# Optimization experiments

Hardware: AMD Instinct MI355X
Metric: run time of the kernel (lower is better)

## Reference

```python
import jax, jax.numpy as jnp
import numpy as np

N = 35          # nodes (hardcoded by x.repeat(35,1,1))
V = 4           # edge views
D1, D2, D3 = 512, 256, 128


def _full_graph_edges():
    # fully connected, no self loops, COO [2, E], E = 35*34
    src, dst = np.meshgrid(np.arange(N), np.arange(N), indexing='ij')
    mask = src != dst
    return np.stack([src[mask], dst[mask]], axis=0).astype(np.int64)


def setup_inputs() -> dict:
    key = jax.random.key(0)
    ks = jax.random.split(key, 8)
    E = N * (N - 1)
    edge_index = jnp.asarray(_full_graph_edges())
    s1, s2, s3 = 1.0 / np.sqrt(V), 1.0 / np.sqrt(V), 1.0 / np.sqrt(V)
    return {
        'x': jnp.ones((N, 1), jnp.float32),
        'edge_attr': jax.random.uniform(ks[0], (E, V), jnp.float32),
        'edge_index': edge_index,
        'mlp1_w': jax.random.normal(ks[1], (V, 1 * D1), jnp.float32) * s1,
        'mlp1_b': jnp.zeros((1 * D1,), jnp.float32),
        'root1': jax.random.normal(ks[2], (1, D1), jnp.float32),
        'bias1': jnp.zeros((D1,), jnp.float32),
        'mlp2_w': jax.random.normal(ks[3], (V, D1 * D2), jnp.float32) * s2,
        'mlp2_b': jnp.zeros((D1 * D2,), jnp.float32),
        'root2': jax.random.normal(ks[4], (D1, D2), jnp.float32) / np.sqrt(D1),
        'bias2': jnp.zeros((D2,), jnp.float32),
        'mlp3_w': jax.random.normal(ks[5], (V, D2 * D3), jnp.float32) * s3,
        'mlp3_b': jnp.zeros((D2 * D3,), jnp.float32),
        'root3': jax.random.normal(ks[6], (D2, D3), jnp.float32) / np.sqrt(D2),
        'bias3': jnp.zeros((D3,), jnp.float32),
    }


def _nnconv(x, edge_attr, src, dst, mlp_w, mlp_b, root, bias, in_c, out_c):
    # edge MLP -> per-edge weight matrix [E, in_c, out_c]
    w = jax.nn.relu(edge_attr @ mlp_w + mlp_b).reshape(-1, in_c, out_c)
    # gather source feats, per-edge matmul: [E, out_c]
    msg = jnp.einsum('ei,eio->eo', x[src], w)
    # scatter-mean to targets
    agg = jax.ops.segment_sum(msg, dst, num_segments=N)
    cnt = jax.ops.segment_sum(jnp.ones_like(msg[:, 0]), dst, num_segments=N)
    agg = agg / jnp.maximum(cnt, 1.0)[:, None]
    return agg + x @ root + bias


def reference(x, edge_attr, edge_index, mlp1_w, mlp1_b, root1, bias1,
              mlp2_w, mlp2_b, root2, bias2, mlp3_w, mlp3_b, root3, bias3):
    src, dst = edge_index[0], edge_index[1]
    h = jax.nn.relu(_nnconv(x, edge_attr, src, dst, mlp1_w, mlp1_b, root1, bias1, 1, D1))
    h = jax.nn.relu(_nnconv(h, edge_attr, src, dst, mlp2_w, mlp2_b, root2, bias2, D1, D2))
    h = jax.nn.relu(_nnconv(h, edge_attr, src, dst, mlp3_w, mlp3_b, root3, bias3, D2, D3))
    # cbt[a, i] = sum_f |h[i, f] - h[a, f]|   (repeat / transpose / abs / sum)
    cbt = jnp.sum(jnp.abs(h[None, :, :] - h[:, None, :]), axis=2)
    return cbt
```

## Files before the change

kernel.cpp:

```cpp
#include <hip/hip_runtime.h>

#define NN 35

typedef float v2f __attribute__((ext_vector_type(2)));

__device__ __forceinline__ v2f pk_fma(v2f a, v2f b, v2f c) {
#if __has_builtin(__builtin_elementwise_fma)
    return __builtin_elementwise_fma(a, b, c);
#else
    v2f d; d.x = fmaf(a.x, b.x, c.x); d.y = fmaf(a.y, b.y, c.y); return d;
#endif
}
__device__ __forceinline__ v2f pk_relu(v2f a) {
    v2f d; d.x = fmaxf(a.x, 0.f); d.y = fmaxf(a.y, 0.f); return d;
}
__device__ __forceinline__ v2f pk_splat(float s) { v2f d; d.x = s; d.y = s; return d; }
__device__ __forceinline__ v2f pk_make(float a, float b) { v2f d; d.x = a; d.y = b; return d; }

__device__ __forceinline__ void agst(float* p, float v) {
    __hip_atomic_store(p, v, __ATOMIC_RELAXED, __HIP_MEMORY_SCOPE_AGENT);
}


__global__ __launch_bounds__(256, 2)
void edge12_kernel(const float* __restrict__ x,
                   const float* __restrict__ ea,
                   const float* __restrict__ W1, const float* __restrict__ b1,
                   const float* __restrict__ root1, const float* __restrict__ bias1,
                   const float* __restrict__ W2, const float* __restrict__ b2,
                   const float* __restrict__ root2,
                   float* __restrict__ part,
                   float* __restrict__ agg3)
{
    const int d  = blockIdx.x;
    const int c  = blockIdx.y;
    const int i0 = c * 8;
    const int o  = threadIdx.x;
    const int bid = c * 35 + d;

    __shared__ __align__(16) float hs[35][8];
    __shared__ float4 as[34];
    __shared__ float xs[NN];

    if (bid < 18) {
        const int zi = bid * 256 + o;
        if (zi < 35 * 128) agst(&agg3[zi], 0.f);
    }

    v2f Wv0[4], Wv1[4], Wv2[4], Wv3[4], BB[4], RR[4];
#pragma unroll
    for (int p = 0; p < 4; ++p) {
        const size_t b0 = (size_t)(i0 + 2 * p) * 256 + o;
        const size_t bq = b0 + 256;
        Wv0[p] = pk_make(W2[b0],          W2[bq]);
        Wv1[p] = pk_make(W2[131072 + b0], W2[131072 + bq]);
        Wv2[p] = pk_make(W2[262144 + b0], W2[262144 + bq]);
        Wv3[p] = pk_make(W2[393216 + b0], W2[393216 + bq]);
        BB[p]  = pk_make(b2[b0],          b2[bq]);
        RR[p]  = pk_make(root2[b0],       root2[bq]);
    }

    if (o < NN) xs[o] = x[o];
    if (o >= 70 && o < 104) {
        const int j = o - 70;
        const int s = j + (j >= d ? 1 : 0);
        as[j] = ((const float4*)ea)[s * 34 + (d < s ? d : d - 1)];
    }
    __syncthreads();

    for (int e = o; e < 280; e += 256) {
        const int s = e >> 3, ii = e & 7, i = i0 + ii;
        const float w0 = W1[i], w1 = W1[512 + i], w2 = W1[1024 + i], w3 = W1[1536 + i];
        const float bb = b1[i];
        float sum = 0.f;
#pragma unroll
        for (int t = 0; t < NN; ++t) {
            if (t == s) continue;
            const float4 a = ((const float4*)ea)[t * 34 + (s < t ? s : s - 1)];
            float w = fmaf(a.x, w0, fmaf(a.y, w1, fmaf(a.z, w2, fmaf(a.w, w3, bb))));
            sum = fmaf(xs[t], fmaxf(w, 0.f), sum);
        }
        hs[s][ii] = fmaxf(sum * (1.f / 34.f) + xs[s] * root1[i] + bias1[i], 0.f);
    }
    __syncthreads();

    v2f acc0 = pk_splat(0.f), acc1 = pk_splat(0.f);
#pragma unroll 2
    for (int j = 0; j < 34; ++j) {
        const int sj = j + (j >= d ? 1 : 0);
        const float4 a = as[j];
        const v2f ax = pk_splat(a.x), ay = pk_splat(a.y);
        const v2f az = pk_splat(a.z), aw = pk_splat(a.w);
#pragma unroll
        for (int k = 0; k < 2; ++k) {
            const float4 hv = ((const float4*)hs[sj])[k];
            {
                const int p = k * 2;
                v2f w = pk_fma(ax, Wv0[p], pk_fma(ay, Wv1[p],
                        pk_fma(az, Wv2[p], pk_fma(aw, Wv3[p], BB[p]))));
                acc0 = pk_fma(pk_make(hv.x, hv.y), pk_relu(w), acc0);
            }
            {
                const int p = k * 2 + 1;
                v2f w = pk_fma(ax, Wv0[p], pk_fma(ay, Wv1[p],
                        pk_fma(az, Wv2[p], pk_fma(aw, Wv3[p], BB[p]))));
                acc1 = pk_fma(pk_make(hv.z, hv.w), pk_relu(w), acc1);
            }
        }
    }
    v2f racc = pk_splat(0.f);
#pragma unroll
    for (int k = 0; k < 2; ++k) {
        const float4 hv = ((const float4*)hs[d])[k];
        racc = pk_fma(pk_make(hv.x, hv.y), RR[k * 2],     racc);
        racc = pk_fma(pk_make(hv.z, hv.w), RR[k * 2 + 1], racc);
    }
    const float acc = acc0.x + acc0.y + acc1.x + acc1.y;
    part[((size_t)(d * 256 + o) << 6) + c] = acc * (1.f / 34.f) + (racc.x + racc.y);
}

__global__ __launch_bounds__(256, 2)
void edge3_kernel(const float* __restrict__ part,
                  const float* __restrict__ bias2,
                  const float* __restrict__ ea,
                  const float* __restrict__ W,
                  const float* __restrict__ bias,
                  const float* __restrict__ root,
                  float* __restrict__ agg)
{
    const int d   = blockIdx.x;
    const int c   = blockIdx.y;
    const int i0  = c * 8;
    const int thr = threadIdx.x;
    const int o   = thr & 127;
    const int g   = thr >> 7;

    __shared__ __align__(16) float hs[35][8];
    __shared__ float4 as[34];

    v2f Wv0[2], Wv1[2], Wv2[2], Wv3[2], BB[2], RR[2];
#pragma unroll
    for (int p = 0; p < 2; ++p) {
        const size_t b0 = (size_t)(i0 + g * 4 + 2 * p) * 128 + o;
        const size_t bq = b0 + 128;
        Wv0[p] = pk_make(W[b0],         W[bq]);
        Wv1[p] = pk_make(W[32768 + b0], W[32768 + bq]);
        Wv2[p] = pk_make(W[65536 + b0], W[65536 + bq]);
        Wv3[p] = pk_make(W[98304 + b0], W[98304 + bq]);
        BB[p]  = pk_make(bias[b0],      bias[bq]);
        RR[p]  = pk_make(root[b0],      root[bq]);
    }

    if (thr < 34) {
        const int s = thr + (thr >= d ? 1 : 0);
        as[thr] = ((const float4*)ea)[s * 34 + (d < s ? d : d - 1)];
    }

    for (int e = thr; e < 280; e += 256) {
        const int s = e >> 3, f = i0 + (e & 7);
        const float4* pp = (const float4*)(part + ((size_t)(s * 256 + f) << 6));
        float4 v0 = pp[0], v1 = pp[1], v2 = pp[2], v3 = pp[3];
#pragma unroll
        for (int q = 4; q < 16; q += 4) {
            const float4 a0 = pp[q], a1 = pp[q + 1], a2 = pp[q + 2], a3 = pp[q + 3];
            v0.x += a0.x; v0.y += a0.y; v0.z += a0.z; v0.w += a0.w;
            v1.x += a1.x; v1.y += a1.y; v1.z += a1.z; v1.w += a1.w;
            v2.x += a2.x; v2.y += a2.y; v2.z += a2.z; v2.w += a2.w;
            v3.x += a3.x; v3.y += a3.y; v3.z += a3.z; v3.w += a3.w;
        }
        const float v = (v0.x + v0.y + v0.z + v0.w) + (v1.x + v1.y + v1.z + v1.w)
                      + (v2.x + v2.y + v2.z + v2.w) + (v3.x + v3.y + v3.z + v3.w);
        hs[s][e & 7] = fmaxf(v + bias2[f], 0.f);
    }
    __syncthreads();

    v2f acc0 = pk_splat(0.f), acc1 = pk_splat(0.f);
#pragma unroll 2
    for (int j = 0; j < 34; ++j) {
        const int sj = j + (j >= d ? 1 : 0);
        const float4 a = as[j];
        const v2f ax = pk_splat(a.x), ay = pk_splat(a.y);
        const v2f az = pk_splat(a.z), aw = pk_splat(a.w);
        const float4 hv = ((const float4*)hs[sj])[g];
        {
            v2f w = pk_fma(ax, Wv0[0], pk_fma(ay, Wv1[0],
                    pk_fma(az, Wv2[0], pk_fma(aw, Wv3[0], BB[0]))));
            acc0 = pk_fma(pk_make(hv.x, hv.y), pk_relu(w), acc0);
        }
        {
            v2f w = pk_fma(ax, Wv0[1], pk_fma(ay, Wv1[1],
                    pk_fma(az, Wv2[1], pk_fma(aw, Wv3[1], BB[1]))));
            acc1 = pk_fma(pk_make(hv.z, hv.w), pk_relu(w), acc1);
        }
    }
    v2f racc = pk_splat(0.f);
    {
        const float4 hv = ((const float4*)hs[d])[g];
        racc = pk_fma(pk_make(hv.x, hv.y), RR[0], racc);
        racc = pk_fma(pk_make(hv.z, hv.w), RR[1], racc);
    }
    const float acc = acc0.x + acc0.y + acc1.x + acc1.y;
    atomicAdd(&agg[d * 128 + o], acc * (1.f / 34.f) + (racc.x + racc.y));
}

__global__ __launch_bounds__(256)
void cbt_kernel(const float* __restrict__ agg3,
                const float* __restrict__ bias3,
                float* __restrict__ out)
{
    const int wv = blockIdx.x * 4 + (threadIdx.x >> 6);
    const int lane = threadIdx.x & 63;
    if (wv >= NN * NN) return;
    const int a_ = wv / NN, i_ = wv % NN;
    float s = 0.f;
#pragma unroll
    for (int q = 0; q < 2; ++q) {
        const int f = lane + q * 64;
        const float bb = bias3[f];
        const float hi = fmaxf(agg3[i_ * 128 + f] + bb, 0.f);
        const float ha = fmaxf(agg3[a_ * 128 + f] + bb, 0.f);
        s += fabsf(hi - ha);
    }
#pragma unroll
    for (int off = 32; off > 0; off >>= 1)
        s += __shfl_xor(s, off, 64);
    if (lane == 0) out[wv] = s;
}

extern "C" void kernel_launch(void* const* d_in, const int* in_sizes, int n_in,
                              void* d_out, int out_size, void* d_ws, size_t ws_size,
                              hipStream_t stream) {
    const float* x      = (const float*)d_in[0];
    const float* ea     = (const float*)d_in[1];
    const float* mlp1_w = (const float*)d_in[3];
    const float* mlp1_b = (const float*)d_in[4];
    const float* root1  = (const float*)d_in[5];
    const float* bias1  = (const float*)d_in[6];
    const float* mlp2_w = (const float*)d_in[7];
    const float* mlp2_b = (const float*)d_in[8];
    const float* root2  = (const float*)d_in[9];
    const float* bias2  = (const float*)d_in[10];
    const float* mlp3_w = (const float*)d_in[11];
    const float* mlp3_b = (const float*)d_in[12];
    const float* root3  = (const float*)d_in[13];
    const float* bias3  = (const float*)d_in[14];
    float* out = (float*)d_out;

    float* ws   = (float*)d_ws;
    float* part = ws;
    float* agg3 = ws + 573440;

    edge12_kernel<<<dim3(NN, 64), 256, 0, stream>>>(
        x, ea, mlp1_w, mlp1_b, root1, bias1, mlp2_w, mlp2_b, root2, part, agg3);
    edge3_kernel<<<dim3(NN, 32), 256, 0, stream>>>(
        part, bias2, ea, mlp3_w, mlp3_b, root3, agg3);
    cbt_kernel<<<(NN * NN + 3) / 4, 256, 0, stream>>>(agg3, bias3, out);
}
```

Measured before the change: 153.8 us.

## Stage edge attrs in shared memory and transpose partial-sum layout

The edge12 kernel now copies the whole edge_attr array (1190 float4) into shared memory once per block. Both the layer-1 recompute and the layer-2 edge loop then read from LDS instead of global memory. The partial-sum buffer is transposed so each block writes a contiguous 256-float row (coalesced). edge3 now reads 64 strided values per output instead of contiguous float4s. This trades coalesced stores for strided gathers on the reduction side and adds about 19KB of LDS per block, which may affect occupancy.

New measurement: 142.8 us. 7.2% less time.

```diff
diff --git a/kernel.cpp b/kernel.cpp
--- a/kernel.cpp
+++ b/kernel.cpp
@@ -38,8 +38,8 @@
     const int o  = threadIdx.x;
     const int bid = c * 35 + d;
 
+    __shared__ __align__(16) float4 eas[1190];
     __shared__ __align__(16) float hs[35][8];
-    __shared__ float4 as[34];
     __shared__ float xs[NN];
 
     if (bid < 18) {
@@ -60,12 +60,8 @@
         RR[p]  = pk_make(root2[b0],       root2[bq]);
     }
 
+    for (int e = o; e < 1190; e += 256) eas[e] = ((const float4*)ea)[e];
     if (o < NN) xs[o] = x[o];
-    if (o >= 70 && o < 104) {
-        const int j = o - 70;
-        const int s = j + (j >= d ? 1 : 0);
-        as[j] = ((const float4*)ea)[s * 34 + (d < s ? d : d - 1)];
-    }
     __syncthreads();
 
     for (int e = o; e < 280; e += 256) {
@@ -76,7 +72,7 @@
 #pragma unroll
         for (int t = 0; t < NN; ++t) {
             if (t == s) continue;
-            const float4 a = ((const float4*)ea)[t * 34 + (s < t ? s : s - 1)];
+            const float4 a = eas[t * 34 + (s < t ? s : s - 1)];
             float w = fmaf(a.x, w0, fmaf(a.y, w1, fmaf(a.z, w2, fmaf(a.w, w3, bb))));
             sum = fmaf(xs[t], fmaxf(w, 0.f), sum);
         }
@@ -88,7 +84,7 @@
 #pragma unroll 2
     for (int j = 0; j < 34; ++j) {
         const int sj = j + (j >= d ? 1 : 0);
-        const float4 a = as[j];
+        const float4 a = eas[sj * 34 + (d < sj ? d : d - 1)];
         const v2f ax = pk_splat(a.x), ay = pk_splat(a.y);
         const v2f az = pk_splat(a.z), aw = pk_splat(a.w);
 #pragma unroll
@@ -116,7 +112,7 @@
         racc = pk_fma(pk_make(hv.z, hv.w), RR[k * 2 + 1], racc);
     }
     const float acc = acc0.x + acc0.y + acc1.x + acc1.y;
-    part[((size_t)(d * 256 + o) << 6) + c] = acc * (1.f / 34.f) + (racc.x + racc.y);
+    part[(size_t)bid * 256 + o] = acc * (1.f / 34.f) + (racc.x + racc.y);
 }
 
 __global__ __launch_bounds__(256, 2)
@@ -157,20 +153,17 @@
     }
 
     for (int e = thr; e < 280; e += 256) {
-        const int s = e >> 3, f = i0 + (e & 7);
-        const float4* pp = (const float4*)(part + ((size_t)(s * 256 + f) << 6));
-        float4 v0 = pp[0], v1 = pp[1], v2 = pp[2], v3 = pp[3];
-#pragma unroll
-        for (int q = 4; q < 16; q += 4) {
-            const float4 a0 = pp[q], a1 = pp[q + 1], a2 = pp[q + 2], a3 = pp[q + 3];
-            v0.x += a0.x; v0.y += a0.y; v0.z += a0.z; v0.w += a0.w;
-            v1.x += a1.x; v1.y += a1.y; v1.z += a1.z; v1.w += a1.w;
-            v2.x += a2.x; v2.y += a2.y; v2.z += a2.z; v2.w += a2.w;
-            v3.x += a3.x; v3.y += a3.y; v3.z += a3.z; v3.w += a3.w;
-        }
-        const float v = (v0.x + v0.y + v0.z + v0.w) + (v1.x + v1.y + v1.z + v1.w)
-                      + (v2.x + v2.y + v2.z + v2.w) + (v3.x + v3.y + v3.z + v3.w);
-        hs[s][e & 7] = fmaxf(v + bias2[f], 0.f);
+        const int s = e >> 3, fi = e & 7, f = i0 + fi;
+        const float* pp = part + s * 256 + f;
+        float s0 = 0.f, s1 = 0.f, s2 = 0.f, s3 = 0.f;
+#pragma unroll
+        for (int cc = 0; cc < 64; cc += 4) {
+            s0 += pp[(size_t)(cc + 0) * 8960];
+            s1 += pp[(size_t)(cc + 1) * 8960];
+            s2 += pp[(size_t)(cc + 2) * 8960];
+            s3 += pp[(size_t)(cc + 3) * 8960];
+        }
+        hs[s][fi] = fmaxf((s0 + s1) + (s2 + s3) + bias2[f], 0.f);
     }
     __syncthreads();
 
```
